# Performance work log

Hardware: AMD Instinct MI355X
Metric: run time of the kernel (lower is better)

## Reference

```python
import jax, jax.numpy as jnp
import numpy as np

B, S, H = 8, 4096, 1024
NUM_WORDS = 8192

def setup_inputs() -> dict:
    key = jax.random.key(0)
    k1, k2 = jax.random.split(key)
    hidden_states = jax.random.normal(k1, (B, S, H), dtype=jnp.float32)
    # contiguous ragged word segments over the flattened token stream,
    # equivalent to per-batch (start, end) word boundaries
    segment_ids = jnp.sort(jax.random.randint(k2, (B * S,), 0, NUM_WORDS)).astype(jnp.int32)
    return {"hidden_states": hidden_states, "segment_ids": segment_ids, "num_segments": NUM_WORDS}

def reference(hidden_states, segment_ids, num_segments):
    # hidden_states: [B, S, H]; segment_ids: [B*S] token -> word id
    tokens = hidden_states.reshape(-1, hidden_states.shape[-1])  # [B*S, H]
    sums = jax.ops.segment_sum(tokens, segment_ids, num_segments=num_segments)  # [W, H]
    counts = jax.ops.segment_sum(jnp.ones((tokens.shape[0],), dtype=tokens.dtype),
                                 segment_ids, num_segments=num_segments)  # [W]
    # average pooling per word; empty segments (count==0) are guarded like the
    # original's `continue` (they would simply not appear; here they are zeros)
    pooled = sums / jnp.maximum(counts, 1.0)[:, None]
    return pooled  # [total_words, H]
```

## Files before the change

### kernel.cpp

```cpp
#include <hip/hip_runtime.h>
#include <hip/hip_bf16.h>


__device__ __forceinline__ int wave_lower_bound(const int* __restrict__ seg,
                                                int n, int val, int lane) {
    int lo = 0;
    int len = n;
    while (len > 64) {
        const int stride = (len + 63) >> 6;
        const int idx = lo + lane * stride;
        const int v = (idx < n) ? seg[idx] : 0x7fffffff;
        const unsigned long long m = __ballot(v < val);
        const int cnt = __popcll(m);
        if (cnt > 0) lo += (cnt - 1) * stride + 1;
        len = stride;
    }
    {
        const int idx = lo + lane;
        const int v = (idx < n) ? seg[idx] : 0x7fffffff;
        const unsigned long long m = __ballot(v < val);
        lo += __popcll(m);
    }
    return lo;
}

__global__ __launch_bounds__(256)
void word_pool_kernel(const float* __restrict__ hs,
                      const int* __restrict__ seg,
                      float* __restrict__ out,
                      int n_tokens, int H, int n_words) {
    __shared__ int bounds[5];

    const int wave = threadIdx.x >> 6;
    const int lane = threadIdx.x & 63;
    const int w0 = blockIdx.x * 4;
    const int w  = w0 + wave;
    if (w >= n_words) return;

    const int start = wave_lower_bound(seg, n_tokens, w, lane);
    if (lane == 0) bounds[wave] = start;
    if (wave == 3) {
        const int b4 = wave_lower_bound(seg, n_tokens, w0 + 4, lane);
        if (lane == 0) bounds[4] = b4;
    }
    __syncthreads();
    const int end = bounds[wave + 1];

    const int c0 = lane * 4;

    float4 acc0 = make_float4(0.f, 0.f, 0.f, 0.f);
    float4 acc1 = acc0, acc2 = acc0, acc3 = acc0;

    for (int t = start; t < end; ++t) {
        const float* row = hs + (size_t)t * H + c0;
        const float4 v0 = *reinterpret_cast<const float4*>(row);
        const float4 v1 = *reinterpret_cast<const float4*>(row + 256);
        const float4 v2 = *reinterpret_cast<const float4*>(row + 512);
        const float4 v3 = *reinterpret_cast<const float4*>(row + 768);
        acc0.x += v0.x; acc0.y += v0.y; acc0.z += v0.z; acc0.w += v0.w;
        acc1.x += v1.x; acc1.y += v1.y; acc1.z += v1.z; acc1.w += v1.w;
        acc2.x += v2.x; acc2.y += v2.y; acc2.z += v2.z; acc2.w += v2.w;
        acc3.x += v3.x; acc3.y += v3.y; acc3.z += v3.z; acc3.w += v3.w;
    }

    const int cnt = end - start;
    const float inv = (cnt > 0) ? (1.0f / (float)cnt) : 0.0f;
    acc0.x *= inv; acc0.y *= inv; acc0.z *= inv; acc0.w *= inv;
    acc1.x *= inv; acc1.y *= inv; acc1.z *= inv; acc1.w *= inv;
    acc2.x *= inv; acc2.y *= inv; acc2.z *= inv; acc2.w *= inv;
    acc3.x *= inv; acc3.y *= inv; acc3.z *= inv; acc3.w *= inv;

    float* orow = out + (size_t)w * H + c0;
    *reinterpret_cast<float4*>(orow)       = acc0;
    *reinterpret_cast<float4*>(orow + 256) = acc1;
    *reinterpret_cast<float4*>(orow + 512) = acc2;
    *reinterpret_cast<float4*>(orow + 768) = acc3;
}

extern "C" void kernel_launch(void* const* d_in, const int* in_sizes, int n_in,
                              void* d_out, int out_size, void* d_ws, size_t ws_size,
                              hipStream_t stream) {
    const float* hs  = (const float*)d_in[0];
    const int*   seg = (const int*)d_in[1];
    float* out = (float*)d_out;

    const int n_tokens = in_sizes[1];
    const int H        = in_sizes[0] / n_tokens;
    const int n_words  = out_size / H;

    dim3 grid((n_words + 3) / 4);
    dim3 block(256);
    word_pool_kernel<<<grid, block, 0, stream>>>(hs, seg, out, n_tokens, H, n_words);
}
```

Measured before the change: 33.59 us.

## Assign four consecutive words per wave and stream segment boundaries inline

Each wave now handles a run of four consecutive words, and each block covers sixteen. Only one binary search per wave is needed, plus one per block for the end bound, instead of one per word. Inside the loop each token's segment id is read to detect word changes, flushing the averaged row and zero-filling empty words. This cuts the binary-search overhead but makes each wave's work serial across four words, with fewer blocks overall. The grid uses n_words/16 with no tail handling, so it assumes n_words is divisible by 16.

```diff
diff --git a/kernel.cpp b/kernel.cpp
--- a/kernel.cpp
+++ b/kernel.cpp
@@ -33,14 +33,13 @@
 
     const int wave = threadIdx.x >> 6;
     const int lane = threadIdx.x & 63;
-    const int w0 = blockIdx.x * 4;
-    const int w  = w0 + wave;
-    if (w >= n_words) return;
+    const int wb0 = blockIdx.x * 16;
+    const int w0  = wb0 + wave * 4;
 
-    const int start = wave_lower_bound(seg, n_tokens, w, lane);
+    const int start = wave_lower_bound(seg, n_tokens, w0, lane);
     if (lane == 0) bounds[wave] = start;
     if (wave == 3) {
-        const int b4 = wave_lower_bound(seg, n_tokens, w0 + 4, lane);
+        const int b4 = wave_lower_bound(seg, n_tokens, wb0 + 16, lane);
         if (lane == 0) bounds[4] = b4;
     }
     __syncthreads();
@@ -50,6 +49,8 @@
 
     float4 acc0 = make_float4(0.f, 0.f, 0.f, 0.f);
     float4 acc1 = acc0, acc2 = acc0, acc3 = acc0;
+    int cur = w0;
+    int cnt = 0;
 
     for (int t = start; t < end; ++t) {
         const float* row = hs + (size_t)t * H + c0;
@@ -57,24 +58,60 @@
         const float4 v1 = *reinterpret_cast<const float4*>(row + 256);
         const float4 v2 = *reinterpret_cast<const float4*>(row + 512);
         const float4 v3 = *reinterpret_cast<const float4*>(row + 768);
+
+        const int s = seg[t];
+        if (s != cur) {
+            const float inv = (cnt > 0) ? (1.0f / (float)cnt) : 0.0f;
+            float* orow = out + (size_t)cur * H + c0;
+            float4 o0 = acc0, o1 = acc1, o2 = acc2, o3 = acc3;
+            o0.x *= inv; o0.y *= inv; o0.z *= inv; o0.w *= inv;
+            o1.x *= inv; o1.y *= inv; o1.z *= inv; o1.w *= inv;
+            o2.x *= inv; o2.y *= inv; o2.z *= inv; o2.w *= inv;
+            o3.x *= inv; o3.y *= inv; o3.z *= inv; o3.w *= inv;
+            *reinterpret_cast<float4*>(orow)       = o0;
+            *reinterpret_cast<float4*>(orow + 256) = o1;
+            *reinterpret_cast<float4*>(orow + 512) = o2;
+            *reinterpret_cast<float4*>(orow + 768) = o3;
+            const float4 z = make_float4(0.f, 0.f, 0.f, 0.f);
+            for (int w = cur + 1; w < s; ++w) {
+                float* zrow = out + (size_t)w * H + c0;
+                *reinterpret_cast<float4*>(zrow)       = z;
+                *reinterpret_cast<float4*>(zrow + 256) = z;
+                *reinterpret_cast<float4*>(zrow + 512) = z;
+                *reinterpret_cast<float4*>(zrow + 768) = z;
+            }
+            acc0 = z; acc1 = z; acc2 = z; acc3 = z;
+            cnt = 0;
+            cur = s;
+        }
+
         acc0.x += v0.x; acc0.y += v0.y; acc0.z += v0.z; acc0.w += v0.w;
         acc1.x += v1.x; acc1.y += v1.y; acc1.z += v1.z; acc1.w += v1.w;
         acc2.x += v2.x; acc2.y += v2.y; acc2.z += v2.z; acc2.w += v2.w;
         acc3.x += v3.x; acc3.y += v3.y; acc3.z += v3.z; acc3.w += v3.w;
+        ++cnt;
     }
 
-    const int cnt = end - start;
-    const float inv = (cnt > 0) ? (1.0f / (float)cnt) : 0.0f;
-    acc0.x *= inv; acc0.y *= inv; acc0.z *= inv; acc0.w *= inv;
-    acc1.x *= inv; acc1.y *= inv; acc1.z *= inv; acc1.w *= inv;
-    acc2.x *= inv; acc2.y *= inv; acc2.z *= inv; acc2.w *= inv;
-    acc3.x *= inv; acc3.y *= inv; acc3.z *= inv; acc3.w *= inv;
-
-    float* orow = out + (size_t)w * H + c0;
-    *reinterpret_cast<float4*>(orow)       = acc0;
-    *reinterpret_cast<float4*>(orow + 256) = acc1;
-    *reinterpret_cast<float4*>(orow + 512) = acc2;
-    *reinterpret_cast<float4*>(orow + 768) = acc3;
+    {
+        const float inv = (cnt > 0) ? (1.0f / (float)cnt) : 0.0f;
+        float* orow = out + (size_t)cur * H + c0;
+        acc0.x *= inv; acc0.y *= inv; acc0.z *= inv; acc0.w *= inv;
+        acc1.x *= inv; acc1.y *= inv; acc1.z *= inv; acc1.w *= inv;
+        acc2.x *= inv; acc2.y *= inv; acc2.z *= inv; acc2.w *= inv;
+        acc3.x *= inv; acc3.y *= inv; acc3.z *= inv; acc3.w *= inv;
+        *reinterpret_cast<float4*>(orow)       = acc0;
+        *reinterpret_cast<float4*>(orow + 256) = acc1;
+        *reinterpret_cast<float4*>(orow + 512) = acc2;
+        *reinterpret_cast<float4*>(orow + 768) = acc3;
+        const float4 z = make_float4(0.f, 0.f, 0.f, 0.f);
+        for (int w = cur + 1; w < w0 + 4; ++w) {
+            float* zrow = out + (size_t)w * H + c0;
+            *reinterpret_cast<float4*>(zrow)       = z;
+            *reinterpret_cast<float4*>(zrow + 256) = z;
+            *reinterpret_cast<float4*>(zrow + 512) = z;
+            *reinterpret_cast<float4*>(zrow + 768) = z;
+        }
+    }
 }
 
 extern "C" void kernel_launch(void* const* d_in, const int* in_sizes, int n_in,
@@ -88,7 +125,7 @@
     const int H        = in_sizes[0] / n_tokens;
     const int n_words  = out_size / H;
 
-    dim3 grid((n_words + 3) / 4);
+    dim3 grid(n_words / 16);
     dim3 block(256);
     word_pool_kernel<<<grid, block, 0, stream>>>(hs, seg, out, n_tokens, H, n_words);
 }
```

Result: no change. 33.94 us (+1.1%).
